# Optimization experiments

Hardware: AMD Instinct MI355X
Metric: run time of the kernel (lower is better)

## Reference

```python
import jax, jax.numpy as jnp
import numpy as np

KS = 3          # deformable kernel size
PAD = 1         # padding (kernel_size // 2)
EPS = 1e-5      # BatchNorm eps


def conv2d(x, w, b):
    # plain 3x3 conv, stride 1, pad 1, NCHW / OIHW
    y = jax.lax.conv_general_dilated(x, w, window_strides=(1, 1),
                                     padding=[(PAD, PAD), (PAD, PAD)],
                                     dimension_numbers=("NCHW", "OIHW", "NCHW"))
    return y + b[None, :, None, None]


def deform_conv(x, offset, mask, w, b):
    # modulated deformable conv v2 (torchvision deform_conv2d semantics)
    B, C, H, W = x.shape
    K = KS * KS
    ky, kx = jnp.meshgrid(jnp.arange(KS), jnp.arange(KS), indexing="ij")
    ky = ky.reshape(-1).astype(x.dtype)
    kx = kx.reshape(-1).astype(x.dtype)
    off = offset.reshape(B, K, 2, H, W)          # channel order: (dy, dx) per kernel tap
    dy, dx = off[:, :, 0], off[:, :, 1]          # [B,K,H,W]
    py = dy + (ky - PAD)[None, :, None, None] + jnp.arange(H, dtype=x.dtype)[None, None, :, None]
    px = dx + (kx - PAD)[None, :, None, None] + jnp.arange(W, dtype=x.dtype)[None, None, None, :]
    y0 = jnp.floor(py); x0 = jnp.floor(px)
    ly = py - y0; lx = px - x0
    y0i = y0.astype(jnp.int32); x0i = x0.astype(jnp.int32)
    y1i = y0i + 1; x1i = x0i + 1
    xf = x.reshape(B, C, H * W)

    def gather(yi, xi):
        valid = (yi >= 0) & (yi < H) & (xi >= 0) & (xi < W)          # zero padding outside
        idx = jnp.clip(yi, 0, H - 1) * W + jnp.clip(xi, 0, W - 1)    # [B,K,H,W]
        g = jax.vmap(lambda xb, ib: jnp.take(xb, ib, axis=1))(xf, idx.reshape(B, -1))
        g = g.reshape(B, C, K, H, W)
        return g * valid[:, None].astype(x.dtype)

    v = (gather(y0i, x0i) * ((1 - ly) * (1 - lx))[:, None]
         + gather(y0i, x1i) * ((1 - ly) * lx)[:, None]
         + gather(y1i, x0i) * (ly * (1 - lx))[:, None]
         + gather(y1i, x1i) * (ly * lx)[:, None])                    # [B,C,K,H,W]
    v = v * mask[:, None]                                            # modulation
    out = jnp.einsum("bckhw,ock->bohw", v, w.reshape(w.shape[0], C, K))
    return out + b[None, :, None, None]


def setup_inputs() -> dict:
    key = jax.random.key(0)
    ks = jax.random.split(key, 5)
    B, Cin, Cout, H, W = 8, 64, 64, 128, 128
    K = KS * KS
    x = jax.random.normal(ks[0], (B, Cin, H, W), jnp.float32)
    off_w = jax.random.normal(ks[1], (2 * K, Cin, KS, KS), jnp.float32) * 0.01
    off_b = jnp.zeros((2 * K,), jnp.float32)
    mod_w = jax.random.normal(ks[2], (K, Cin, KS, KS), jnp.float32) * 0.01
    mod_b = jnp.zeros((K,), jnp.float32)
    w = jax.random.normal(ks[3], (Cout, Cin, KS, KS), jnp.float32) * (1.0 / np.sqrt(Cin * K))
    b = jnp.zeros((Cout,), jnp.float32)
    gamma = jnp.ones((Cout,), jnp.float32)
    beta = jnp.zeros((Cout,), jnp.float32)
    return {"x": x, "off_w": off_w, "off_b": off_b, "mod_w": mod_w,
            "mod_b": mod_b, "w": w, "b": b, "gamma": gamma, "beta": beta}


def reference(x, off_w, off_b, mod_w, mod_b, w, b, gamma, beta):
    offset = conv2d(x, off_w, off_b)                       # [B,2K,H,W]
    mask = 2.0 * jax.nn.sigmoid(conv2d(x, mod_w, mod_b))   # [B,K,H,W]
    y = deform_conv(x, offset, mask, w, b)                 # [B,Cout,H,W]
    # BatchNorm2d (training-mode batch stats, biased variance)
    mean = y.mean(axis=(0, 2, 3), keepdims=True)
    var = y.var(axis=(0, 2, 3), keepdims=True)
    yn = (y - mean) / jnp.sqrt(var + EPS)
    yn = gamma[None, :, None, None] * yn + beta[None, :, None, None]
    return jax.nn.relu(yn)
```

## Files before the change

kernel.cpp:

```cpp
#include <hip/hip_runtime.h>
#include <math.h>

#define Hn 128
#define Wn 128
#define HW 16384
#define NPIX 131072
#define EPSv 1e-5f

#define XT_OFF   0
#define OFF_OFF  4194304
#define MASK_OFF 6553600
#define WBTA_OFF 7733248
#define WBTB_OFF 7743488
#define STAT_OFF 7763968


typedef short s16x8 __attribute__((ext_vector_type(8)));
typedef unsigned short u16x4 __attribute__((ext_vector_type(4)));
typedef float f32x4 __attribute__((ext_vector_type(4)));

__device__ __forceinline__ unsigned short f2bf(float f) {
  unsigned u = __float_as_uint(f);
  return (unsigned short)((u + 0x7fffu + ((u >> 16) & 1u)) >> 16);
}
__device__ __forceinline__ float bf2f(unsigned short s) {
  return __uint_as_float((unsigned)s << 16);
}

__global__ __launch_bounds__(256) void prep_kernel(
    const float* __restrict__ off_w, const float* __restrict__ mod_w,
    const float* __restrict__ w, unsigned short* __restrict__ wbtA,
    unsigned short* __restrict__ wbtB, float* __restrict__ stat) {
  int i = blockIdx.x * 256 + threadIdx.x;
  if (i < 128) stat[i] = 0.f;
  if (i < 20480) {
    int e = i & 31, oc = (i >> 5) & 31, it = i >> 10;
    int tp = it % 5, chunk = it / 5;
    int tap = tp * 2 + (e >> 4);
    int c = (chunk << 4) + (e & 15);
    float v = 0.f;
    if (tap < 9) {
      if (oc < 18) v = off_w[(oc * 64 + c) * 9 + tap];
      else if (oc < 27) v = mod_w[((oc - 18) * 64 + c) * 9 + tap];
    }
    wbtA[i] = f2bf(v);
  } else if (i < 20480 + 40960) {
    int j = i - 20480;
    int e = j & 31, oc = (j >> 5) & 63, it = j >> 11;
    int tp = it % 5, chunk = it / 5;
    int tap = tp * 2 + (e >> 4);
    int c = (chunk << 4) + (e & 15);
    float v = (tap < 9) ? w[(oc * 64 + c) * 9 + tap] : 0.f;
    wbtB[j] = f2bf(v);
  }
}

__global__ __launch_bounds__(256) void xform_kernel(
    const float* __restrict__ x, unsigned short* __restrict__ xt) {
  int blk = blockIdx.x;
  int b = blk & 7;
  int hw = ((blk >> 3) << 8) + threadIdx.x;
  const float* xb = x + ((size_t)(b << 6) << 14) + hw;
  unsigned short* o = xt + (((size_t)(b << 14)) + hw) * 64;
#pragma unroll
  for (int g = 0; g < 8; ++g) {
    float v[8];
#pragma unroll
    for (int j = 0; j < 8; ++j) v[j] = xb[(size_t)((g << 3) + j) << 14];
    s16x8 pk;
#pragma unroll
    for (int j = 0; j < 8; ++j) pk[j] = (short)f2bf(v[j]);
    *(s16x8*)(o + (g << 3)) = pk;
  }
}

__global__ __launch_bounds__(256, 4) void convA_mfma_kernel(
    const unsigned short* __restrict__ xt, const unsigned short* __restrict__ wbtA,
    const float* __restrict__ off_b, const float* __restrict__ mod_b,
    float* __restrict__ off_out, float* __restrict__ mask_out) {
  int t = threadIdx.x;
  int bx = blockIdx.x;
  int b = bx & 7, h = bx >> 3;
  int ln = t & 15, quad = (t >> 4) & 3, wv = t >> 6;
  int p0 = (wv << 5) + ln, p1 = p0 + 16;
  int s_ = quad >> 1, cj = (quad & 1) << 3;

  f32x4 acc[2][2];
#pragma unroll
  for (int mt = 0; mt < 2; ++mt)
#pragma unroll
    for (int nt = 0; nt < 2; ++nt) acc[mt][nt] = (f32x4){0.f, 0.f, 0.f, 0.f};

  const unsigned short* xtb = xt + ((size_t)(b << 14)) * 64;

#pragma unroll 5
  for (int it = 0; it < 20; ++it) {
    int chunk = it / 5, tp = it - chunk * 5;
    int tap = tp * 2 + s_;
    s16x8 B0 = (s16x8){0, 0, 0, 0, 0, 0, 0, 0};
    s16x8 B1 = (s16x8){0, 0, 0, 0, 0, 0, 0, 0};
    if (tap < 9) {
      int gy = h + tap / 3 - 1;
      if (gy >= 0 && gy < Hn) {
        const unsigned short* rowp = xtb + ((size_t)(gy << 7)) * 64 + (chunk << 4) + cj;
        int gx0 = p0 + tap % 3 - 1;
        int gx1 = p1 + tap % 3 - 1;
        if (gx0 >= 0 && gx0 < Wn) B0 = *(const s16x8*)(rowp + (gx0 << 6));
        if (gx1 >= 0 && gx1 < Wn) B1 = *(const s16x8*)(rowp + (gx1 << 6));
      }
    }
#pragma unroll
    for (int mt = 0; mt < 2; ++mt) {
      s16x8 A = *(const s16x8*)(wbtA + (size_t)((it << 5) + (mt << 4) + ln) * 32 + (quad << 3));
      acc[mt][0] = __builtin_amdgcn_mfma_f32_16x16x32_bf16(A, B0, acc[mt][0], 0, 0, 0);
      acc[mt][1] = __builtin_amdgcn_mfma_f32_16x16x32_bf16(A, B1, acc[mt][1], 0, 0, 0);
    }
  }

  int hw = h << 7;
#pragma unroll
  for (int mt = 0; mt < 2; ++mt)
#pragma unroll
    for (int r = 0; r < 4; ++r) {
      int oc = (mt << 4) + (quad << 2) + r;
#pragma unroll
      for (int nt = 0; nt < 2; ++nt) {
        int px = (wv << 5) + (nt << 4) + ln;
        float val = acc[mt][nt][r];
        if (oc < 18) {
          off_out[(((size_t)b * 18 + oc) << 14) + hw + px] = val + off_b[oc];
        } else if (oc < 27) {
          float z = val + mod_b[oc - 18];
          mask_out[(((size_t)b * 9 + (oc - 18)) << 14) + hw + px] = 2.f / (1.f + expf(-z));
        }
      }
    }
}

__global__ __launch_bounds__(256, 3) void deform_mfma_kernel(
    const unsigned short* __restrict__ xt, const float* __restrict__ off,
    const float* __restrict__ mask, const unsigned short* __restrict__ wbtB,
    const float* __restrict__ bias, float* __restrict__ y) {
  __shared__ short vlds[2 * 128 * 40];
  __shared__ unsigned short geow[9 * 128 * 4];
  __shared__ unsigned short geoi[9 * 128];
  int t = threadIdx.x;
  int bx = blockIdx.x;
  int b = bx & 7, h = bx >> 3;
  int lane = t & 63, wv = t >> 6;
  int l4 = lane & 15, quad = (lane >> 4) & 3;
  int pb = (wv << 5) + (lane & 31);
  int halfb = lane >> 5;
  int hw = h << 7;

  for (int i = t; i < 1152; i += 256) {
    int tap = i >> 7, p2 = i & 127;
    int ob = ((b * 18 + 2 * tap) << 14) + hw + p2;
    float dy = off[ob];
    float dx = off[ob + HW];
    float m = mask[((b * 9 + tap) << 14) + hw + p2];
    float py = dy + (float)(h + tap / 3 - 1);
    float pxf = dx + (float)(p2 + tap % 3 - 1);
    float y0f = floorf(py), x0f = floorf(pxf);
    float ly = py - y0f, lx = pxf - x0f;
    int y0 = (int)y0f, x0 = (int)x0f;
    int y1 = y0 + 1, x1 = x0 + 1;
    float fy0 = (y0 >= 0 && y0 < Hn) ? 1.f : 0.f;
    float fy1 = (y1 >= 0 && y1 < Hn) ? 1.f : 0.f;
    float fx0 = (x0 >= 0 && x0 < Wn) ? 1.f : 0.f;
    float fx1 = (x1 >= 0 && x1 < Wn) ? 1.f : 0.f;
    float ax0 = (1.f - lx) * fx0, ax1 = lx * fx1;
    float ay0 = (1.f - ly) * fy0 * m, ay1 = ly * fy1 * m;
    int cy0 = min(max(y0, 0), Hn - 1), cy1 = min(max(y1, 0), Hn - 1);
    int cx0 = min(max(x0, 0), Wn - 1), cx1 = min(max(x1, 0), Wn - 1);
    int cbase = min(cx0, Wn - 2), rbase = min(cy0, Hn - 2);
    float gx0 = (cx0 == cbase ? ax0 : 0.f) + (cx1 == cbase ? ax1 : 0.f);
    float gx1 = (cx0 == cbase + 1 ? ax0 : 0.f) + (cx1 == cbase + 1 ? ax1 : 0.f);
    float gy0 = (cy0 == rbase ? ay0 : 0.f) + (cy1 == rbase ? ay1 : 0.f);
    float gy1 = (cy0 == rbase + 1 ? ay0 : 0.f) + (cy1 == rbase + 1 ? ay1 : 0.f);
    unsigned short* gw = geow + i * 4;
    gw[0] = f2bf(gy0);
    gw[1] = f2bf(gy1);
    gw[2] = f2bf(gx0);
    gw[3] = f2bf(gx1);
    geoi[i] = (unsigned short)((rbase << 7) + cbase);
  }
  __syncthreads();

  f32x4 acc[4][2];
#pragma unroll
  for (int mt = 0; mt < 4; ++mt)
#pragma unroll
    for (int nt = 0; nt < 2; ++nt) acc[mt][nt] = (f32x4){0.f, 0.f, 0.f, 0.f};

  const unsigned short* xtb = xt + ((size_t)(b << 14)) * 64;

#pragma unroll 2
  for (int it = 0; it < 20; ++it) {
    int chunk = it / 5, tp = it - chunk * 5;
    int ch0 = (chunk << 4) + (halfb << 3);
    float gy0[2], gy1[2], gx0[2], gx1[2];
    const unsigned short* cp[2];
#pragma unroll
    for (int s = 0; s < 2; ++s) {
      int tap = tp * 2 + s;
      if (tap < 9) {
        int gidx = (tap << 7) + pb;
        u16x4 wq = *(const u16x4*)(geow + gidx * 4);
        unsigned ib = geoi[gidx];
        gy0[s] = bf2f(wq[0]);
        gy1[s] = bf2f(wq[1]);
        gx0[s] = bf2f(wq[2]);
        gx1[s] = bf2f(wq[3]);
        cp[s] = xtb + ((size_t)ib) * 64 + ch0;
      } else {
        cp[s] = xtb + ch0;
        gy0[s] = gy1[s] = gx0[s] = gx1[s] = 0.f;
      }
    }
    s16x8 c00[2], c01[2], c10[2], c11[2];
#pragma unroll
    for (int s = 0; s < 2; ++s) {
      int tap = tp * 2 + s;
      if (tap < 9) {
        c00[s] = *(const s16x8*)(cp[s]);
        c01[s] = *(const s16x8*)(cp[s] + 64);
        c10[s] = *(const s16x8*)(cp[s] + 8192);
        c11[s] = *(const s16x8*)(cp[s] + 8192 + 64);
      }
    }
    s16x8 pk[2];
#pragma unroll
    for (int s = 0; s < 2; ++s) {
      int tap = tp * 2 + s;
      if (tap < 9) {
#pragma unroll
        for (int j = 0; j < 8; ++j) {
          float v = gy0[s] * (gx0[s] * bf2f((unsigned short)c00[s][j]) +
                              gx1[s] * bf2f((unsigned short)c01[s][j])) +
                    gy1[s] * (gx0[s] * bf2f((unsigned short)c10[s][j]) +
                              gx1[s] * bf2f((unsigned short)c11[s][j]));
          pk[s][j] = (short)f2bf(v);
        }
      } else {
#pragma unroll
        for (int j = 0; j < 8; ++j) pk[s][j] = 0;
      }
    }
    short* vd = vlds + (it & 1) * 5120 + pb * 40 + (halfb << 3);
    *(s16x8*)(vd) = pk[0];
    *(s16x8*)(vd + 16) = pk[1];
    const short* vb = vlds + (it & 1) * 5120;
    s16x8 B0 = *(const s16x8*)(vb + ((wv << 5) + l4) * 40 + (quad << 3));
    s16x8 B1 = *(const s16x8*)(vb + ((wv << 5) + 16 + l4) * 40 + (quad << 3));
#pragma unroll
    for (int mt = 0; mt < 4; ++mt) {
      s16x8 A = *(const s16x8*)(wbtB + (size_t)((it << 6) + (mt << 4) + l4) * 32 + (quad << 3));
      acc[mt][0] = __builtin_amdgcn_mfma_f32_16x16x32_bf16(A, B0, acc[mt][0], 0, 0, 0);
      acc[mt][1] = __builtin_amdgcn_mfma_f32_16x16x32_bf16(A, B1, acc[mt][1], 0, 0, 0);
    }
  }

#pragma unroll
  for (int mt = 0; mt < 4; ++mt)
#pragma unroll
    for (int r = 0; r < 4; ++r) {
      int oc = (mt << 4) + (quad << 2) + r;
      float bv = bias[oc];
      float* yp = y + (((size_t)(b << 6) + oc) << 14) + hw;
      yp[(wv << 5) + l4] = acc[mt][0][r] + bv;
      yp[(wv << 5) + 16 + l4] = acc[mt][1][r] + bv;
    }
}

__global__ __launch_bounds__(256) void stats2_kernel(
    const float* __restrict__ y, float* __restrict__ stat) {
  int bxx = blockIdx.x;
  int c = bxx & 63, sl = bxx >> 6;
  int bb = sl >> 1;
  const float4* yp = (const float4*)(y + (((size_t)bb * 64 + c) << 14) + ((sl & 1) << 13));
  float s = 0.f, ss = 0.f;
  for (int i = threadIdx.x; i < 2048; i += 256) {
    float4 v = yp[i];
    s += v.x + v.y + v.z + v.w;
    ss += v.x * v.x + v.y * v.y + v.z * v.z + v.w * v.w;
  }
#pragma unroll
  for (int o = 32; o > 0; o >>= 1) {
    s += __shfl_xor(s, o);
    ss += __shfl_xor(ss, o);
  }
  __shared__ float shs[4], shss[4];
  int lane = threadIdx.x & 63, wv = threadIdx.x >> 6;
  if (lane == 0) { shs[wv] = s; shss[wv] = ss; }
  __syncthreads();
  if (threadIdx.x == 0) {
    float S = shs[0] + shs[1] + shs[2] + shs[3];
    float SS = shss[0] + shss[1] + shss[2] + shss[3];
    atomicAdd(stat + c, S);
    atomicAdd(stat + 64 + c, SS);
  }
}

__global__ __launch_bounds__(256) void bnrelu_kernel(
    float* __restrict__ y, const float* __restrict__ stat,
    const float* __restrict__ gamma, const float* __restrict__ beta) {
  float4* y4 = (float4*)y;
  for (int i = blockIdx.x * 256 + threadIdx.x; i < 2097152; i += gridDim.x * 256) {
    int c = (i >> 12) & 63;
    float mean = stat[c] * (1.f / (float)NPIX);
    float var = stat[64 + c] * (1.f / (float)NPIX) - mean * mean;
    float r = rsqrtf(var + EPSv);
    float g = gamma[c] * r;
    float bt = beta[c] - mean * g;
    float4 v = y4[i];
    v.x = fmaxf(v.x * g + bt, 0.f);
    v.y = fmaxf(v.y * g + bt, 0.f);
    v.z = fmaxf(v.z * g + bt, 0.f);
    v.w = fmaxf(v.w * g + bt, 0.f);
    y4[i] = v;
  }
}

extern "C" void kernel_launch(void* const* d_in, const int* in_sizes, int n_in,
                              void* d_out, int out_size, void* d_ws, size_t ws_size,
                              hipStream_t stream) {
  const float* x     = (const float*)d_in[0];
  const float* off_w = (const float*)d_in[1];
  const float* off_b = (const float*)d_in[2];
  const float* mod_w = (const float*)d_in[3];
  const float* mod_b = (const float*)d_in[4];
  const float* w     = (const float*)d_in[5];
  const float* b     = (const float*)d_in[6];
  const float* gamma = (const float*)d_in[7];
  const float* beta  = (const float*)d_in[8];
  float* out = (float*)d_out;
  float* ws  = (float*)d_ws;

  unsigned short* xt  = (unsigned short*)(ws + XT_OFF);
  float* offo  = ws + OFF_OFF;
  float* masko = ws + MASK_OFF;
  unsigned short* wbtA = (unsigned short*)(ws + WBTA_OFF);
  unsigned short* wbtB = (unsigned short*)(ws + WBTB_OFF);
  float* stat  = ws + STAT_OFF;

  prep_kernel<<<240, 256, 0, stream>>>(off_w, mod_w, w, wbtA, wbtB, stat);
  xform_kernel<<<512, 256, 0, stream>>>(x, xt);
  convA_mfma_kernel<<<1024, 256, 0, stream>>>(xt, wbtA, off_b, mod_b, offo, masko);
  deform_mfma_kernel<<<1024, 256, 0, stream>>>(xt, offo, masko, wbtB, b, out);
  stats2_kernel<<<1024, 256, 0, stream>>>(out, stat);
  bnrelu_kernel<<<8192, 256, 0, stream>>>(out, stat, gamma, beta);
}
```

Baseline: 245.5 us.

## Feed sampled values directly as MFMA A operand, drop LDS staging

The deform kernel now builds the bilinearly sampled activations directly in registers in MFMA A-operand layout (pixels as rows), with weights pre-packed in per-lane B-fragment order. This removes the LDS double buffer and its write/read round trip. The loop is reordered so per-tap geometry is loaded once and reused across the four channel chunks. Output stores become float4 per lane. Occupancy hint rises to 4 blocks per SM. Trade-off: each lane now gathers for 16 pixels per MFMA tile, which may change the gather access pattern.

```diff
diff --git a/kernel.cpp b/kernel.cpp
--- a/kernel.cpp
+++ b/kernel.cpp
@@ -46,10 +46,14 @@
     wbtA[i] = f2bf(v);
   } else if (i < 20480 + 40960) {
     int j = i - 20480;
-    int e = j & 31, oc = (j >> 5) & 63, it = j >> 11;
+    int j3 = j & 7;
+    int l = (j >> 3) & 63;
+    int nt = (j >> 9) & 3;
+    int it = j >> 11;
     int tp = it % 5, chunk = it / 5;
-    int tap = tp * 2 + (e >> 4);
-    int c = (chunk << 4) + (e & 15);
+    int tap = tp * 2 + (l >> 5);
+    int c = (chunk << 4) + (((l >> 4) & 1) << 3) + j3;
+    int oc = (nt << 4) + (l & 15);
     float v = (tap < 9) ? w[(oc * 64 + c) * 9 + tap] : 0.f;
     wbtB[j] = f2bf(v);
   }
@@ -137,20 +141,20 @@
     }
 }
 
-__global__ __launch_bounds__(256, 3) void deform_mfma_kernel(
+__global__ __launch_bounds__(256, 4) void deform_mfma_kernel(
     const unsigned short* __restrict__ xt, const float* __restrict__ off,
     const float* __restrict__ mask, const unsigned short* __restrict__ wbtB,
     const float* __restrict__ bias, float* __restrict__ y) {
-  __shared__ short vlds[2 * 128 * 40];
   __shared__ unsigned short geow[9 * 128 * 4];
   __shared__ unsigned short geoi[9 * 128];
   int t = threadIdx.x;
   int bx = blockIdx.x;
   int b = bx & 7, h = bx >> 3;
   int lane = t & 63, wv = t >> 6;
-  int l4 = lane & 15, quad = (lane >> 4) & 3;
-  int pb = (wv << 5) + (lane & 31);
-  int halfb = lane >> 5;
+  int l4 = lane & 15;
+  int s4 = lane >> 4;
+  int tapS = lane >> 5;
+  int chalf = s4 & 1;
   int hw = h << 7;
 
   for (int i = t; i < 1152; i += 256) {
@@ -187,90 +191,86 @@
   }
   __syncthreads();
 
-  f32x4 acc[4][2];
-#pragma unroll
-  for (int mt = 0; mt < 4; ++mt)
-#pragma unroll
-    for (int nt = 0; nt < 2; ++nt) acc[mt][nt] = (f32x4){0.f, 0.f, 0.f, 0.f};
+  f32x4 acc[2][4];
+#pragma unroll
+  for (int m = 0; m < 2; ++m)
+#pragma unroll
+    for (int n = 0; n < 4; ++n) acc[m][n] = (f32x4){0.f, 0.f, 0.f, 0.f};
 
   const unsigned short* xtb = xt + ((size_t)(b << 14)) * 64;
 
-#pragma unroll 2
-  for (int it = 0; it < 20; ++it) {
-    int chunk = it / 5, tp = it - chunk * 5;
-    int ch0 = (chunk << 4) + (halfb << 3);
+  for (int tp = 0; tp < 5; ++tp) {
+    int tap = tp * 2 + tapS;
+    bool live = (tap < 9);
     float gy0[2], gy1[2], gx0[2], gx1[2];
-    const unsigned short* cp[2];
-#pragma unroll
-    for (int s = 0; s < 2; ++s) {
-      int tap = tp * 2 + s;
-      if (tap < 9) {
-        int gidx = (tap << 7) + pb;
+    const unsigned short* cpb[2];
+#pragma unroll
+    for (int m = 0; m < 2; ++m) {
+      if (live) {
+        int px = (wv << 5) + (m << 4) + l4;
+        int gidx = (tap << 7) + px;
         u16x4 wq = *(const u16x4*)(geow + gidx * 4);
         unsigned ib = geoi[gidx];
-        gy0[s] = bf2f(wq[0]);
-        gy1[s] = bf2f(wq[1]);
-        gx0[s] = bf2f(wq[2]);
-        gx1[s] = bf2f(wq[3]);
-        cp[s] = xtb + ((size_t)ib) * 64 + ch0;
+        gy0[m] = bf2f(wq[0]);
+        gy1[m] = bf2f(wq[1]);
+        gx0[m] = bf2f(wq[2]);
+        gx1[m] = bf2f(wq[3]);
+        cpb[m] = xtb + (size_t)ib * 64 + (chalf << 3);
       } else {
-        cp[s] = xtb + ch0;
-        gy0[s] = gy1[s] = gx0[s] = gx1[s] = 0.f;
-      }
-    }
-    s16x8 c00[2], c01[2], c10[2], c11[2];
-#pragma unroll
-    for (int s = 0; s < 2; ++s) {
-      int tap = tp * 2 + s;
-      if (tap < 9) {
-        c00[s] = *(const s16x8*)(cp[s]);
-        c01[s] = *(const s16x8*)(cp[s] + 64);
-        c10[s] = *(const s16x8*)(cp[s] + 8192);
-        c11[s] = *(const s16x8*)(cp[s] + 8192 + 64);
-      }
-    }
-    s16x8 pk[2];
-#pragma unroll
-    for (int s = 0; s < 2; ++s) {
-      int tap = tp * 2 + s;
-      if (tap < 9) {
-#pragma unroll
-        for (int j = 0; j < 8; ++j) {
-          float v = gy0[s] * (gx0[s] * bf2f((unsigned short)c00[s][j]) +
-                              gx1[s] * bf2f((unsigned short)c01[s][j])) +
-                    gy1[s] * (gx0[s] * bf2f((unsigned short)c10[s][j]) +
-                              gx1[s] * bf2f((unsigned short)c11[s][j]));
-          pk[s][j] = (short)f2bf(v);
+        cpb[m] = xtb;
+        gy0[m] = gy1[m] = gx0[m] = gx1[m] = 0.f;
+      }
+    }
+#pragma unroll 2
+    for (int chunk = 0; chunk < 4; ++chunk) {
+      int it = chunk * 5 + tp;
+      s16x8 A[2];
+#pragma unroll
+      for (int m = 0; m < 2; ++m) {
+        if (live) {
+          const unsigned short* cp = cpb[m] + (chunk << 4);
+          s16x8 c00 = *(const s16x8*)(cp);
+          s16x8 c01 = *(const s16x8*)(cp + 64);
+          s16x8 c10 = *(const s16x8*)(cp + 8192);
+          s16x8 c11 = *(const s16x8*)(cp + 8192 + 64);
+#pragma unroll
+          for (int j = 0; j < 8; ++j) {
+            float v = gy0[m] * (gx0[m] * bf2f((unsigned short)c00[j]) +
+                                gx1[m] * bf2f((unsigned short)c01[j])) +
+                      gy1[m] * (gx0[m] * bf2f((unsigned short)c10[j]) +
+                                gx1[m] * bf2f((unsigned short)c11[j]));
+            A[m][j] = (short)f2bf(v);
+          }
+        } else {
+#pragma unroll
+          for (int j = 0; j < 8; ++j) A[m][j] = 0;
         }
-      } else {
-#pragma unroll
-        for (int j = 0; j < 8; ++j) pk[s][j] = 0;
-      }
-    }
-    short* vd = vlds + (it & 1) * 5120 + pb * 40 + (halfb << 3);
-    *(s16x8*)(vd) = pk[0];
-    *(s16x8*)(vd + 16) = pk[1];
-    const short* vb = vlds + (it & 1) * 5120;
-    s16x8 B0 = *(const s16x8*)(vb + ((wv << 5) + l4) * 40 + (quad << 3));
-    s16x8 B1 = *(const s16x8*)(vb + ((wv << 5) + 16 + l4) * 40 + (quad << 3));
-#pragma unroll
-    for (int mt = 0; mt < 4; ++mt) {
-      s16x8 A = *(const s16x8*)(wbtB + (size_t)((it << 6) + (mt << 4) + l4) * 32 + (quad << 3));
-      acc[mt][0] = __builtin_amdgcn_mfma_f32_16x16x32_bf16(A, B0, acc[mt][0], 0, 0, 0);
-      acc[mt][1] = __builtin_amdgcn_mfma_f32_16x16x32_bf16(A, B1, acc[mt][1], 0, 0, 0);
-    }
-  }
-
-#pragma unroll
-  for (int mt = 0; mt < 4; ++mt)
-#pragma unroll
-    for (int r = 0; r < 4; ++r) {
-      int oc = (mt << 4) + (quad << 2) + r;
+      }
+      const unsigned short* wb = wbtB + (((size_t)it) << 11) + (lane << 3);
+#pragma unroll
+      for (int n = 0; n < 4; ++n) {
+        s16x8 Bf = *(const s16x8*)(wb + (n << 9));
+        acc[0][n] = __builtin_amdgcn_mfma_f32_16x16x32_bf16(A[0], Bf, acc[0][n], 0, 0, 0);
+        acc[1][n] = __builtin_amdgcn_mfma_f32_16x16x32_bf16(A[1], Bf, acc[1][n], 0, 0, 0);
+      }
+    }
+  }
+
+#pragma unroll
+  for (int m = 0; m < 2; ++m) {
+    int px0 = (wv << 5) + (m << 4) + (s4 << 2);
+#pragma unroll
+    for (int n = 0; n < 4; ++n) {
+      int oc = (n << 4) + l4;
       float bv = bias[oc];
-      float* yp = y + (((size_t)(b << 6) + oc) << 14) + hw;
-      yp[(wv << 5) + l4] = acc[mt][0][r] + bv;
-      yp[(wv << 5) + 16 + l4] = acc[mt][1][r] + bv;
-    }
+      float4 o;
+      o.x = acc[m][n][0] + bv;
+      o.y = acc[m][n][1] + bv;
+      o.z = acc[m][n][2] + bv;
+      o.w = acc[m][n][3] + bv;
+      *(float4*)(y + (((size_t)(b << 6) + oc) << 14) + hw + px0) = o;
+    }
+  }
 }
 
 __global__ __launch_bounds__(256) void stats2_kernel(
```

Result: faster. 233.6 us (-4.9%).
